# Optimization experiments

Hardware: AMD Instinct MI355X
Metric: run time of the kernel (lower is better)

## Reference

```python
import jax, jax.numpy as jnp
import numpy as np

B, N, S, NS, D = 8, 16384, 1024, 64, 128
RADIUS = 0.2
CH = [131, 128, 128, 256]  # mlp_spec after use_xyz: 128+3 input channels
EPS = 1e-5


def setup_inputs() -> dict:
    key = jax.random.key(0)
    ks = jax.random.split(key, 16)
    inp = {}
    inp["xyz"] = jax.random.uniform(ks[0], (B, N, 3), dtype=jnp.float32)
    inp["points"] = jax.random.normal(ks[1], (B, D, N), dtype=jnp.float32)
    inp["fps_idx"] = jax.random.randint(ks[2], (B, S), 0, N, dtype=jnp.int32)
    for i in range(3):
        cin, cout = CH[i], CH[i + 1]
        inp[f"W{i}"] = jax.random.normal(ks[3 + 4 * i], (cout, cin), dtype=jnp.float32) * np.float32(1.0 / np.sqrt(cin))
        inp[f"b{i}"] = jnp.zeros((cout,), dtype=jnp.float32)
        inp[f"g{i}"] = jnp.ones((cout,), dtype=jnp.float32)
        inp[f"be{i}"] = jnp.zeros((cout,), dtype=jnp.float32)
    return inp


def _ball_query(xyz, new_xyz):
    # squared distances [B, S, N] (expanded-form, same math as square_distance)
    d = (jnp.sum(new_xyz ** 2, -1, keepdims=True)
         + jnp.sum(xyz ** 2, -1)[:, None, :]
         - 2.0 * jnp.einsum('bsc,bnc->bsn', new_xyz, xyz))
    ar = jnp.arange(N, dtype=jnp.int32)[None, None, :]
    idx = jnp.where(d > RADIUS ** 2, N, ar)          # out-of-ball -> sentinel N
    idx = jnp.sort(idx, axis=-1)[:, :, :NS]          # global sort emulating top-k
    idx = jnp.where(idx == N, idx[:, :, :1], idx)    # pad with first valid neighbor
    return idx


def reference(xyz, points, fps_idx, W0, b0, g0, be0, W1, b1, g1, be1, W2, b2, g2, be2):
    feats = points.transpose(0, 2, 1)  # [B, N, D]
    new_xyz = jnp.take_along_axis(xyz, fps_idx[..., None], axis=1)  # [B, S, 3]
    idx = _ball_query(xyz, new_xyz)  # [B, S, NS]

    gather = jax.vmap(lambda a, i: a[i])  # per-batch fancy gather
    grouped_xyz = gather(xyz, idx) - new_xyz[:, :, None, :]   # [B, S, NS, 3]
    grouped_pts = gather(feats, idx)                          # [B, S, NS, D]
    x = jnp.concatenate([grouped_xyz, grouped_pts], axis=-1)  # [B, S, NS, 131]

    # SharedMLP: 1x1 Conv2d + BatchNorm (training-mode stats) + ReLU
    for W, b, g, be in ((W0, b0, g0, be0), (W1, b1, g1, be1), (W2, b2, g2, be2)):
        x = jnp.einsum('bsnc,oc->bsno', x, W) + b
        m = jnp.mean(x, axis=(0, 1, 2))
        v = jnp.var(x, axis=(0, 1, 2))
        x = jax.nn.relu(g * (x - m) * jax.lax.rsqrt(v + EPS) + be)

    new_features = jnp.max(x, axis=2).transpose(0, 2, 1)  # max over nsample -> [B, C', S]
    return new_xyz, new_features, fps_idx
```

## Files before the change

kernel.cpp:

```cpp
#include <hip/hip_runtime.h>
#include <hip/hip_bf16.h>

#define BB 8
#define NN 16384
#define SS 1024
#define NSMP 64
#define DD 128
#define R2 0.04f
#define EPSV 1e-5f

typedef _Float16 half2t __attribute__((ext_vector_type(2)));
typedef _Float16 half8t __attribute__((ext_vector_type(8)));

#define O_PT    0ull
#define O_Y0    33554432ull
#define O_Y1    167772160ull
#define O_IDX   301989888ull
#define O_MAXB  304087040ull
#define O_MINB  312475648ull
#define O_W0T   320864256ull
#define O_W1T   320931328ull
#define O_W2T   320996864ull
#define O_PS0   321127936ull
#define O_PQ0   321259008ull
#define O_PS1   321390080ull
#define O_PQ1   321521152ull
#define O_PS2   321652224ull
#define O_PQ2   321914368ull
#define O_SC0   322176512ull
#define O_SH0   322177024ull
#define O_SC1   322177536ull
#define O_SH1   322178048ull
#define O_SC2   322178560ull
#define O_SH2   322179584ull
#define WS_NEEDED 322180608ull
#define PART_BYTES 1048576ull

#define OUT_XYZ 0
#define OUT_FEAT 24576
#define OUT_FPS (24576 + 2097152)

__global__ __launch_bounds__(256) void k_transpose_pts(const float* __restrict__ pts,
                                                       _Float16* __restrict__ ptsT) {
  __shared__ float tile[32][33];
  int b = blockIdx.z;
  int n0 = blockIdx.x * 32, c0 = blockIdx.y * 32;
  int tx = threadIdx.x, ty = threadIdx.y;
#pragma unroll
  for (int k = 0; k < 4; k++) {
    int c = c0 + ty + k * 8;
    tile[ty + k * 8][tx] = pts[((size_t)b * DD + c) * NN + n0 + tx];
  }
  __syncthreads();
#pragma unroll
  for (int k = 0; k < 4; k++) {
    int n = n0 + ty + k * 8;
    ptsT[((size_t)b * NN + n) * DD + c0 + tx] = (_Float16)tile[tx][ty + k * 8];
  }
}

__global__ __launch_bounds__(256) void k_wt(const float* __restrict__ W0, const float* __restrict__ W1,
                                            const float* __restrict__ W2, float* __restrict__ W0t,
                                            float* __restrict__ W1t, float* __restrict__ W2t) {
  int id = blockIdx.x * 256 + threadIdx.x;
  if (id < 131 * 128) {
    int c = id >> 7, o = id & 127;
    int c0 = (c < 128) ? (c + 3) : (c - 128);
    W0t[id] = W0[o * 131 + c0];
  } else if (id < 131 * 128 + 128 * 128) {
    int j = id - 131 * 128;
    int c = j >> 7, o = j & 127;
    W1t[j] = W1[o * 128 + c];
  } else if (id < 131 * 128 + 128 * 128 + 128 * 256) {
    int j = id - (131 * 128 + 128 * 128);
    int c = j >> 8, o = j & 255;
    W2t[j] = W2[o * 128 + c];
  }
}

__global__ __launch_bounds__(256) void k_newxyz(const float* __restrict__ xyz, const int* __restrict__ fps,
                                                float* __restrict__ out) {
  int id = blockIdx.x * 256 + threadIdx.x;
  int fi = fps[id];
  int b = id >> 10;
  const float* p = xyz + ((size_t)b * NN + fi) * 3;
  float* o = out + OUT_XYZ + (size_t)id * 3;
  o[0] = p[0]; o[1] = p[1]; o[2] = p[2];
  out[OUT_FPS + id] = (float)fi;
}

__global__ __launch_bounds__(256) void k_ballq(const float* __restrict__ xyz, const int* __restrict__ fps,
                                               int* __restrict__ idxb) {
  int w = (blockIdx.x * 256 + threadIdx.x) >> 6;
  int lane = threadIdx.x & 63;
  int b = w >> 10;
  int fi = fps[w];
  const float* cp = xyz + ((size_t)b * NN + fi) * 3;
  float cx = cp[0], cy = cp[1], cz = cp[2];
  float A = __fadd_rn(__fadd_rn(__fmul_rn(cx, cx), __fmul_rn(cy, cy)), __fmul_rn(cz, cz));
  const float* xb = xyz + (size_t)b * NN * 3;
  int cnt = 0, firstn = -1;
  int* myidx = idxb + (size_t)w * NSMP;
  for (int nb = 0; nb < NN && cnt < NSMP; nb += 64) {
    int n = nb + lane;
    float px = xb[n * 3], py = xb[n * 3 + 1], pz = xb[n * 3 + 2];
    float Bv = __fadd_rn(__fadd_rn(__fmul_rn(px, px), __fmul_rn(py, py)), __fmul_rn(pz, pz));
    float dot = __fadd_rn(__fadd_rn(__fmul_rn(cx, px), __fmul_rn(cy, py)), __fmul_rn(cz, pz));
    float d = __fsub_rn(__fadd_rn(A, Bv), __fmul_rn(2.0f, dot));
    bool valid = !(d > R2);
    unsigned long long mask = __ballot(valid);
    if (firstn < 0 && mask) firstn = nb + __builtin_ctzll(mask);
    int prefix = __popcll(mask & ((1ull << lane) - 1ull));
    int pos = cnt + prefix;
    if (valid && pos < NSMP) myidx[pos] = n;
    cnt += __popcll(mask);
    if (cnt > NSMP) cnt = NSMP;
  }
  if (lane >= cnt) myidx[lane] = firstn;
}

__global__ __launch_bounds__(256, 2) void k_mlp0(const float* __restrict__ xyz,
                                                 const _Float16* __restrict__ ptsT,
                                                 const int* __restrict__ fps, const int* __restrict__ idxb,
                                                 const float* __restrict__ W0t, const float* __restrict__ b0,
                                                 _Float16* __restrict__ y0, float* __restrict__ psum,
                                                 float* __restrict__ psq) {
  __shared__ float xs[64 * 133];
  __shared__ float rbuf[128 * 2];
  __shared__ int smidx[64];
  __shared__ float smc[3];
  int t = threadIdx.x;
  int bs = blockIdx.x;
  int b = bs >> 10;
  if (t < 64) smidx[t] = idxb[(size_t)bs * 64 + t];
  if (t < 3) {
    int fi = fps[bs];
    smc[t] = xyz[((size_t)b * NN + fi) * 3 + t];
  }
  __syncthreads();
  {
    int row = t >> 2, q = t & 3;
    int n = smidx[row];
    const half8t* src = (const half8t*)(ptsT + ((size_t)b * NN + n) * DD);
#pragma unroll
    for (int i = 0; i < 4; i++) {
      int j = q + i * 4;
      half8t v = src[j];
      float* dstp = xs + row * 133 + j * 8;
#pragma unroll
      for (int k = 0; k < 8; k++) dstp[k] = (float)v[k];
    }
  }
  if (t < 64) {
    int n = smidx[t];
    const float* p = xyz + ((size_t)b * NN + n) * 3;
    xs[t * 133 + 128] = p[0] - smc[0];
    xs[t * 133 + 129] = p[1] - smc[1];
    xs[t * 133 + 130] = p[2] - smc[2];
  }
  __syncthreads();
  int p = t & 63;
  int obase = __builtin_amdgcn_readfirstlane((t >> 6) * 32);
  float acc[32];
#pragma unroll
  for (int oi = 0; oi < 32; oi++) acc[oi] = b0[obase + oi];
#pragma unroll 2
  for (int c = 0; c < 131; c++) {
    float xv = xs[p * 133 + c];
    const float* wr = W0t + c * 128 + obase;
#pragma unroll
    for (int oi = 0; oi < 32; oi++) acc[oi] = fmaf(xv, wr[oi], acc[oi]);
  }
  __syncthreads();
#pragma unroll
  for (int oi = 0; oi < 32; oi++) xs[p * 133 + obase + oi] = acc[oi];
  __syncthreads();
  {
    _Float16* dst = y0 + (size_t)bs * 8192;
#pragma unroll
    for (int i = 0; i < 16; i++) {
      int flat = i * 512 + 2 * t;
      int row = flat >> 7, col = flat & 127;
      half2t h;
      h[0] = (_Float16)xs[row * 133 + col];
      h[1] = (_Float16)xs[row * 133 + col + 1];
      *(half2t*)(dst + flat) = h;
    }
  }
  {
    int col = t & 127, half = t >> 7;
    float s = 0.f, q = 0.f;
#pragma unroll 4
    for (int r = half * 32; r < half * 32 + 32; r++) {
      float v = xs[r * 133 + col];
      s += v;
      q = fmaf(v, v, q);
    }
    if (half) { rbuf[col * 2] = s; rbuf[col * 2 + 1] = q; }
    __syncthreads();
    if (!half) {
      s += rbuf[col * 2];
      q += rbuf[col * 2 + 1];
      int slot = bs & 255;
      atomicAdd(&psum[col * 256 + slot], s);
      atomicAdd(&psq[col * 256 + slot], q);
    }
  }
}

__global__ __launch_bounds__(256, 2) void k_mlp1(const _Float16* __restrict__ y0,
                                                 const float* __restrict__ sc, const float* __restrict__ sh,
                                                 const float* __restrict__ W1t, const float* __restrict__ b1,
                                                 _Float16* __restrict__ y1, float* __restrict__ psum,
                                                 float* __restrict__ psq) {
  __shared__ float xs[64 * 133];
  __shared__ float rbuf[128 * 2];
  int t = threadIdx.x;
  int bs = blockIdx.x;
  {
    int colb = (2 * t) & 127;
    float a0 = sc[colb], a1 = sc[colb + 1];
    float c0 = sh[colb], c1 = sh[colb + 1];
    const _Float16* src = y0 + (size_t)bs * 8192;
#pragma unroll
    for (int i = 0; i < 16; i++) {
      int flat = i * 512 + 2 * t;
      int row = flat >> 7, col = flat & 127;
      half2t h = *(const half2t*)(src + flat);
      xs[row * 133 + col] = fmaxf(fmaf((float)h[0], a0, c0), 0.f);
      xs[row * 133 + col + 1] = fmaxf(fmaf((float)h[1], a1, c1), 0.f);
    }
  }
  __syncthreads();
  int p = t & 63;
  int obase = __builtin_amdgcn_readfirstlane((t >> 6) * 32);
  float acc[32];
#pragma unroll
  for (int oi = 0; oi < 32; oi++) acc[oi] = b1[obase + oi];
#pragma unroll 2
  for (int c = 0; c < 128; c++) {
    float xv = xs[p * 133 + c];
    const float* wr = W1t + c * 128 + obase;
#pragma unroll
    for (int oi = 0; oi < 32; oi++) acc[oi] = fmaf(xv, wr[oi], acc[oi]);
  }
  __syncthreads();
#pragma unroll
  for (int oi = 0; oi < 32; oi++) xs[p * 133 + obase + oi] = acc[oi];
  __syncthreads();
  {
    _Float16* dst = y1 + (size_t)bs * 8192;
#pragma unroll
    for (int i = 0; i < 16; i++) {
      int flat = i * 512 + 2 * t;
      int row = flat >> 7, col = flat & 127;
      half2t h;
      h[0] = (_Float16)xs[row * 133 + col];
      h[1] = (_Float16)xs[row * 133 + col + 1];
      *(half2t*)(dst + flat) = h;
    }
  }
  {
    int col = t & 127, half = t >> 7;
    float s = 0.f, q = 0.f;
#pragma unroll 4
    for (int r = half * 32; r < half * 32 + 32; r++) {
      float v = xs[r * 133 + col];
      s += v;
      q = fmaf(v, v, q);
    }
    if (half) { rbuf[col * 2] = s; rbuf[col * 2 + 1] = q; }
    __syncthreads();
    if (!half) {
      s += rbuf[col * 2];
      q += rbuf[col * 2 + 1];
      int slot = bs & 255;
      atomicAdd(&psum[col * 256 + slot], s);
      atomicAdd(&psq[col * 256 + slot], q);
    }
  }
}

__global__ __launch_bounds__(256, 2) void k_mlp2(const _Float16* __restrict__ y1,
                                                 const float* __restrict__ sc, const float* __restrict__ sh,
                                                 const float* __restrict__ W2t, const float* __restrict__ b2,
                                                 float* __restrict__ maxb, float* __restrict__ minb,
                                                 float* __restrict__ psum, float* __restrict__ psq) {
  __shared__ float xs[64 * 133];
  __shared__ float rbuf[128 * 4];
  int t = threadIdx.x;
  int bs = blockIdx.x;
  {
    int colb = (2 * t) & 127;
    float a0 = sc[colb], a1 = sc[colb + 1];
    float c0 = sh[colb], c1 = sh[colb + 1];
    const _Float16* src = y1 + (size_t)bs * 8192;
#pragma unroll
    for (int i = 0; i < 16; i++) {
      int flat = i * 512 + 2 * t;
      int row = flat >> 7, col = flat & 127;
      half2t h = *(const half2t*)(src + flat);
      xs[row * 133 + col] = fmaxf(fmaf((float)h[0], a0, c0), 0.f);
      xs[row * 133 + col + 1] = fmaxf(fmaf((float)h[1], a1, c1), 0.f);
    }
  }
  __syncthreads();
  int p = t & 63;
  int og = t >> 6;
  int obase = __builtin_amdgcn_readfirstlane(og * 64);
  float acc[64];
#pragma unroll
  for (int j = 0; j < 64; j++) acc[j] = b2[obase + j];
  for (int c = 0; c < 128; c++) {
    float xv = xs[p * 133 + c];
    const float* wr = W2t + c * 256 + obase;
#pragma unroll
    for (int j = 0; j < 64; j++) acc[j] = fmaf(xv, wr[j], acc[j]);
  }
  __syncthreads();
  for (int ph = 0; ph < 2; ph++) {
    if ((og >> 1) == ph) {
#pragma unroll
      for (int j = 0; j < 64; j++) {
        int colw = (obase + j) & 127;
        xs[p * 133 + colw] = acc[j];
      }
    }
    __syncthreads();
    {
      int col = t & 127, half = t >> 7;
      float s = 0.f, q = 0.f, mx = -3.4e38f, mn = 3.4e38f;
#pragma unroll 4
      for (int r = half * 32; r < half * 32 + 32; r++) {
        float v = xs[r * 133 + col];
        s += v;
        q = fmaf(v, v, q);
        mx = fmaxf(mx, v);
        mn = fminf(mn, v);
      }
      if (half) {
        rbuf[col * 4] = s; rbuf[col * 4 + 1] = q;
        rbuf[col * 4 + 2] = mx; rbuf[col * 4 + 3] = mn;
      }
      __syncthreads();
      if (!half) {
        s += rbuf[col * 4];
        q += rbuf[col * 4 + 1];
        mx = fmaxf(mx, rbuf[col * 4 + 2]);
        mn = fminf(mn, rbuf[col * 4 + 3]);
        int o = ph * 128 + col;
        maxb[(size_t)bs * 256 + o] = mx;
        minb[(size_t)bs * 256 + o] = mn;
        int slot = bs & 255;
        atomicAdd(&psum[o * 256 + slot], s);
        atomicAdd(&psq[o * 256 + slot], q);
      }
    }
    __syncthreads();
  }
}

__global__ __launch_bounds__(256) void k_fin(const float* __restrict__ psum, const float* __restrict__ psq,
                                             const float* __restrict__ g, const float* __restrict__ be,
                                             float* __restrict__ sc, float* __restrict__ sh, int nch) {
  int o = threadIdx.x;
  if (o >= nch) return;
  float s = 0.f, q = 0.f;
  for (int k = 0; k < 256; k++) {
    s += psum[o * 256 + k];
    q += psq[o * 256 + k];
  }
  const float inv = 1.0f / 524288.0f;
  float m = s * inv;
  float ey2 = q * inv;
  float v = fmaf(-m, m, ey2);
  v = fmaxf(v, 0.f);
  float r = rsqrtf(v + EPSV);
  float a = g[o] * r;
  sc[o] = a;
  sh[o] = fmaf(-m, a, be[o]);
}

__global__ __launch_bounds__(256) void k_out(const float* __restrict__ maxb, const float* __restrict__ minb,
                                             const float* __restrict__ sc, const float* __restrict__ sh,
                                             float* __restrict__ out) {
  int flat = blockIdx.x * 256 + threadIdx.x;
  int b = flat >> 18;
  int o = (flat >> 10) & 255;
  int s = flat & 1023;
  float a = sc[o], c_ = sh[o];
  size_t mi = ((size_t)(b * 1024 + s)) * 256 + o;
  float v = (a >= 0.f) ? maxb[mi] : minb[mi];
  out[OUT_FEAT + flat] = fmaxf(fmaf(a, v, c_), 0.f);
}

extern "C" void kernel_launch(void* const* d_in, const int* in_sizes, int n_in,
                              void* d_out, int out_size, void* d_ws, size_t ws_size,
                              hipStream_t stream) {
  const float* xyz = (const float*)d_in[0];
  const float* pts = (const float*)d_in[1];
  const int* fps = (const int*)d_in[2];
  const float* W0 = (const float*)d_in[3];
  const float* b0 = (const float*)d_in[4];
  const float* g0 = (const float*)d_in[5];
  const float* be0 = (const float*)d_in[6];
  const float* W1 = (const float*)d_in[7];
  const float* b1 = (const float*)d_in[8];
  const float* g1 = (const float*)d_in[9];
  const float* be1 = (const float*)d_in[10];
  const float* W2 = (const float*)d_in[11];
  const float* b2 = (const float*)d_in[12];
  const float* g2 = (const float*)d_in[13];
  const float* be2 = (const float*)d_in[14];
  float* out = (float*)d_out;
  char* ws = (char*)d_ws;

  k_newxyz<<<32, 256, 0, stream>>>(xyz, fps, out);
  if (ws_size < WS_NEEDED) return;

  _Float16* ptsT = (_Float16*)(ws + O_PT);
  _Float16* y0 = (_Float16*)(ws + O_Y0);
  _Float16* y1 = (_Float16*)(ws + O_Y1);
  int* idxb = (int*)(ws + O_IDX);
  float* maxbf = (float*)(ws + O_MAXB);
  float* minbf = (float*)(ws + O_MINB);
  float* W0t = (float*)(ws + O_W0T);
  float* W1t = (float*)(ws + O_W1T);
  float* W2t = (float*)(ws + O_W2T);
  float* ps0 = (float*)(ws + O_PS0);
  float* pq0 = (float*)(ws + O_PQ0);
  float* ps1 = (float*)(ws + O_PS1);
  float* pq1 = (float*)(ws + O_PQ1);
  float* ps2 = (float*)(ws + O_PS2);
  float* pq2 = (float*)(ws + O_PQ2);
  float* sc0 = (float*)(ws + O_SC0);
  float* sh0 = (float*)(ws + O_SH0);
  float* sc1 = (float*)(ws + O_SC1);
  float* sh1 = (float*)(ws + O_SH1);
  float* sc2 = (float*)(ws + O_SC2);
  float* sh2 = (float*)(ws + O_SH2);

  hipMemsetAsync(ws + O_PS0, 0, PART_BYTES, stream);
  k_transpose_pts<<<dim3(NN / 32, DD / 32, BB), dim3(32, 8), 0, stream>>>(pts, ptsT);
  k_wt<<<258, 256, 0, stream>>>(W0, W1, W2, W0t, W1t, W2t);
  k_ballq<<<2048, 256, 0, stream>>>(xyz, fps, idxb);
  k_mlp0<<<8192, 256, 0, stream>>>(xyz, ptsT, fps, idxb, W0t, b0, y0, ps0, pq0);
  k_fin<<<1, 256, 0, stream>>>(ps0, pq0, g0, be0, sc0, sh0, 128);
  k_mlp1<<<8192, 256, 0, stream>>>(y0, sc0, sh0, W1t, b1, y1, ps1, pq1);
  k_fin<<<1, 256, 0, stream>>>(ps1, pq1, g1, be1, sc1, sh1, 128);
  k_mlp2<<<8192, 256, 0, stream>>>(y1, sc1, sh1, W2t, b2, maxbf, minbf, ps2, pq2);
  k_fin<<<1, 256, 0, stream>>>(ps2, pq2, g2, be2, sc2, sh2, 256);
  k_out<<<8192, 256, 0, stream>>>(maxbf, minbf, sc2, sh2, out);
}
```

Measured before the change: 114.6 us.

## Use fp16 MFMA matrix instructions for the three pointwise MLP layers

Replaces the scalar fp32 FMA loops in the three MLP layers with 16x16x32 fp16 MFMA instructions. Activations are staged in LDS as fp16 and the weights are pre-converted to padded fp16 row-major buffers. The three xyz channels of the first layer are handled with a scalar fix-up after the MFMA part. This is meant to cut the compute-bound FMA cost, at the price of lower precision on activations, weights and the relative xyz coordinates, plus extra LDS use.

```diff
diff --git a/kernel.cpp b/kernel.cpp
--- a/kernel.cpp
+++ b/kernel.cpp
@@ -11,6 +11,7 @@
 
 typedef _Float16 half2t __attribute__((ext_vector_type(2)));
 typedef _Float16 half8t __attribute__((ext_vector_type(8)));
+typedef float f32x4 __attribute__((ext_vector_type(4)));
 
 #define O_PT    0ull
 #define O_Y0    33554432ull
@@ -60,21 +61,26 @@
 }
 
 __global__ __launch_bounds__(256) void k_wt(const float* __restrict__ W0, const float* __restrict__ W1,
-                                            const float* __restrict__ W2, float* __restrict__ W0t,
-                                            float* __restrict__ W1t, float* __restrict__ W2t) {
+                                            const float* __restrict__ W2, _Float16* __restrict__ W0h,
+                                            _Float16* __restrict__ W1h, _Float16* __restrict__ W2h) {
   int id = blockIdx.x * 256 + threadIdx.x;
-  if (id < 131 * 128) {
-    int c = id >> 7, o = id & 127;
-    int c0 = (c < 128) ? (c + 3) : (c - 128);
-    W0t[id] = W0[o * 131 + c0];
-  } else if (id < 131 * 128 + 128 * 128) {
-    int j = id - 131 * 128;
-    int c = j >> 7, o = j & 127;
-    W1t[j] = W1[o * 128 + c];
-  } else if (id < 131 * 128 + 128 * 128 + 128 * 256) {
-    int j = id - (131 * 128 + 128 * 128);
-    int c = j >> 8, o = j & 255;
-    W2t[j] = W2[o * 128 + c];
+  const int T0 = 128 * 136, T1 = 128 * 136, T2 = 256 * 136;
+  if (id < T0) {
+    int o = id / 136, c = id % 136;
+    float v = 0.f;
+    if (c < 131) {
+      int c0 = (c < 128) ? (c + 3) : (c - 128);
+      v = W0[o * 131 + c0];
+    }
+    W0h[id] = (_Float16)v;
+  } else if (id < T0 + T1) {
+    int j = id - T0;
+    int o = j / 136, c = j % 136;
+    W1h[j] = (_Float16)((c < 128) ? W1[o * 128 + c] : 0.f);
+  } else if (id < T0 + T1 + T2) {
+    int j = id - T0 - T1;
+    int o = j / 136, c = j % 136;
+    W2h[j] = (_Float16)((c < 128) ? W2[o * 128 + c] : 0.f);
   }
 }
 
@@ -122,9 +128,10 @@
 __global__ __launch_bounds__(256, 2) void k_mlp0(const float* __restrict__ xyz,
                                                  const _Float16* __restrict__ ptsT,
                                                  const int* __restrict__ fps, const int* __restrict__ idxb,
-                                                 const float* __restrict__ W0t, const float* __restrict__ b0,
+                                                 const _Float16* __restrict__ W0h, const float* __restrict__ b0,
                                                  _Float16* __restrict__ y0, float* __restrict__ psum,
                                                  float* __restrict__ psq) {
+  __shared__ _Float16 xh[64 * 136];
   __shared__ float xs[64 * 133];
   __shared__ float rbuf[128 * 2];
   __shared__ int smidx[64];
@@ -145,35 +152,62 @@
 #pragma unroll
     for (int i = 0; i < 4; i++) {
       int j = q + i * 4;
-      half8t v = src[j];
-      float* dstp = xs + row * 133 + j * 8;
-#pragma unroll
-      for (int k = 0; k < 8; k++) dstp[k] = (float)v[k];
+      *(half8t*)(xh + row * 136 + j * 8) = src[j];
     }
   }
   if (t < 64) {
     int n = smidx[t];
     const float* p = xyz + ((size_t)b * NN + n) * 3;
-    xs[t * 133 + 128] = p[0] - smc[0];
-    xs[t * 133 + 129] = p[1] - smc[1];
-    xs[t * 133 + 130] = p[2] - smc[2];
-  }
-  __syncthreads();
-  int p = t & 63;
-  int obase = __builtin_amdgcn_readfirstlane((t >> 6) * 32);
-  float acc[32];
-#pragma unroll
-  for (int oi = 0; oi < 32; oi++) acc[oi] = b0[obase + oi];
-#pragma unroll 2
-  for (int c = 0; c < 131; c++) {
-    float xv = xs[p * 133 + c];
-    const float* wr = W0t + c * 128 + obase;
-#pragma unroll
-    for (int oi = 0; oi < 32; oi++) acc[oi] = fmaf(xv, wr[oi], acc[oi]);
-  }
-  __syncthreads();
-#pragma unroll
-  for (int oi = 0; oi < 32; oi++) xs[p * 133 + obase + oi] = acc[oi];
+    xh[t * 136 + 128] = (_Float16)(p[0] - smc[0]);
+    xh[t * 136 + 129] = (_Float16)(p[1] - smc[1]);
+    xh[t * 136 + 130] = (_Float16)(p[2] - smc[2]);
+  }
+  __syncthreads();
+  int lane = t & 63;
+  int m0 = __builtin_amdgcn_readfirstlane((t >> 6) * 16);
+  int lr = lane & 15, lk = lane >> 4;
+  half8t afr[4];
+#pragma unroll
+  for (int kt = 0; kt < 4; kt++)
+    afr[kt] = *(const half8t*)(xh + (m0 + lr) * 136 + kt * 32 + lk * 8);
+  f32x4 acc[8];
+#pragma unroll
+  for (int nt = 0; nt < 8; nt++) {
+    float bv = b0[nt * 16 + lr];
+    f32x4 cv = {bv, bv, bv, bv};
+    acc[nt] = cv;
+  }
+#pragma unroll
+  for (int kt = 0; kt < 4; kt++) {
+#pragma unroll
+    for (int nt = 0; nt < 8; nt++) {
+      half8t bw = *(const half8t*)(W0h + (nt * 16 + lr) * 136 + kt * 32 + lk * 8);
+      acc[nt] = __builtin_amdgcn_mfma_f32_16x16x32_f16(afr[kt], bw, acc[nt], 0, 0, 0);
+    }
+  }
+  {
+    float xr[4][3];
+#pragma unroll
+    for (int r = 0; r < 4; r++) {
+      int m = m0 + lk * 4 + r;
+      xr[r][0] = (float)xh[m * 136 + 128];
+      xr[r][1] = (float)xh[m * 136 + 129];
+      xr[r][2] = (float)xh[m * 136 + 130];
+    }
+#pragma unroll
+    for (int nt = 0; nt < 8; nt++) {
+      const _Float16* wp = W0h + (nt * 16 + lr) * 136 + 128;
+      float w0 = (float)wp[0], w1 = (float)wp[1], w2 = (float)wp[2];
+#pragma unroll
+      for (int r = 0; r < 4; r++)
+        acc[nt][r] += xr[r][0] * w0 + xr[r][1] * w1 + xr[r][2] * w2;
+    }
+  }
+#pragma unroll
+  for (int nt = 0; nt < 8; nt++)
+#pragma unroll
+    for (int r = 0; r < 4; r++)
+      xs[(m0 + lk * 4 + r) * 133 + nt * 16 + lr] = acc[nt][r];
   __syncthreads();
   {
     _Float16* dst = y0 + (size_t)bs * 8192;
@@ -210,9 +244,10 @@
 
 __global__ __launch_bounds__(256, 2) void k_mlp1(const _Float16* __restrict__ y0,
                                                  const float* __restrict__ sc, const float* __restrict__ sh,
-                                                 const float* __restrict__ W1t, const float* __restrict__ b1,
+                                                 const _Float16* __restrict__ W1h, const float* __restrict__ b1,
                                                  _Float16* __restrict__ y1, float* __restrict__ psum,
                                                  float* __restrict__ psq) {
+  __shared__ _Float16 xh[64 * 136];
   __shared__ float xs[64 * 133];
   __shared__ float rbuf[128 * 2];
   int t = threadIdx.x;
@@ -227,26 +262,40 @@
       int flat = i * 512 + 2 * t;
       int row = flat >> 7, col = flat & 127;
       half2t h = *(const half2t*)(src + flat);
-      xs[row * 133 + col] = fmaxf(fmaf((float)h[0], a0, c0), 0.f);
-      xs[row * 133 + col + 1] = fmaxf(fmaf((float)h[1], a1, c1), 0.f);
-    }
-  }
-  __syncthreads();
-  int p = t & 63;
-  int obase = __builtin_amdgcn_readfirstlane((t >> 6) * 32);
-  float acc[32];
-#pragma unroll
-  for (int oi = 0; oi < 32; oi++) acc[oi] = b1[obase + oi];
-#pragma unroll 2
-  for (int c = 0; c < 128; c++) {
-    float xv = xs[p * 133 + c];
-    const float* wr = W1t + c * 128 + obase;
-#pragma unroll
-    for (int oi = 0; oi < 32; oi++) acc[oi] = fmaf(xv, wr[oi], acc[oi]);
-  }
-  __syncthreads();
-#pragma unroll
-  for (int oi = 0; oi < 32; oi++) xs[p * 133 + obase + oi] = acc[oi];
+      half2t o;
+      o[0] = (_Float16)fmaxf(fmaf((float)h[0], a0, c0), 0.f);
+      o[1] = (_Float16)fmaxf(fmaf((float)h[1], a1, c1), 0.f);
+      *(half2t*)(xh + row * 136 + col) = o;
+    }
+  }
+  __syncthreads();
+  int lane = t & 63;
+  int m0 = __builtin_amdgcn_readfirstlane((t >> 6) * 16);
+  int lr = lane & 15, lk = lane >> 4;
+  half8t afr[4];
+#pragma unroll
+  for (int kt = 0; kt < 4; kt++)
+    afr[kt] = *(const half8t*)(xh + (m0 + lr) * 136 + kt * 32 + lk * 8);
+  f32x4 acc[8];
+#pragma unroll
+  for (int nt = 0; nt < 8; nt++) {
+    float bv = b1[nt * 16 + lr];
+    f32x4 cv = {bv, bv, bv, bv};
+    acc[nt] = cv;
+  }
+#pragma unroll
+  for (int kt = 0; kt < 4; kt++) {
+#pragma unroll
+    for (int nt = 0; nt < 8; nt++) {
+      half8t bw = *(const half8t*)(W1h + (nt * 16 + lr) * 136 + kt * 32 + lk * 8);
+      acc[nt] = __builtin_amdgcn_mfma_f32_16x16x32_f16(afr[kt], bw, acc[nt], 0, 0, 0);
+    }
+  }
+#pragma unroll
+  for (int nt = 0; nt < 8; nt++)
+#pragma unroll
+    for (int r = 0; r < 4; r++)
+      xs[(m0 + lk * 4 + r) * 133 + nt * 16 + lr] = acc[nt][r];
   __syncthreads();
   {
     _Float16* dst = y1 + (size_t)bs * 8192;
@@ -283,9 +332,10 @@
 
 __global__ __launch_bounds__(256, 2) void k_mlp2(const _Float16* __restrict__ y1,
                                                  const float* __restrict__ sc, const float* __restrict__ sh,
-                                                 const float* __restrict__ W2t, const float* __restrict__ b2,
+                                                 const _Float16* __restrict__ W2h, const float* __restrict__ b2,
                                                  float* __restrict__ maxb, float* __restrict__ minb,
                                                  float* __restrict__ psum, float* __restrict__ psq) {
+  __shared__ _Float16 xh[64 * 136];
   __shared__ float xs[64 * 133];
   __shared__ float rbuf[128 * 4];
   int t = threadIdx.x;
@@ -300,32 +350,41 @@
       int flat = i * 512 + 2 * t;
       int row = flat >> 7, col = flat & 127;
       half2t h = *(const half2t*)(src + flat);
-      xs[row * 133 + col] = fmaxf(fmaf((float)h[0], a0, c0), 0.f);
-      xs[row * 133 + col + 1] = fmaxf(fmaf((float)h[1], a1, c1), 0.f);
-    }
-  }
-  __syncthreads();
-  int p = t & 63;
-  int og = t >> 6;
-  int obase = __builtin_amdgcn_readfirstlane(og * 64);
-  float acc[64];
-#pragma unroll
-  for (int j = 0; j < 64; j++) acc[j] = b2[obase + j];
-  for (int c = 0; c < 128; c++) {
-    float xv = xs[p * 133 + c];
-    const float* wr = W2t + c * 256 + obase;
-#pragma unroll
-    for (int j = 0; j < 64; j++) acc[j] = fmaf(xv, wr[j], acc[j]);
-  }
-  __syncthreads();
+      half2t o;
+      o[0] = (_Float16)fmaxf(fmaf((float)h[0], a0, c0), 0.f);
+      o[1] = (_Float16)fmaxf(fmaf((float)h[1], a1, c1), 0.f);
+      *(half2t*)(xh + row * 136 + col) = o;
+    }
+  }
+  __syncthreads();
+  int lane = t & 63;
+  int m0 = __builtin_amdgcn_readfirstlane((t >> 6) * 16);
+  int lr = lane & 15, lk = lane >> 4;
+  half8t afr[4];
+#pragma unroll
+  for (int kt = 0; kt < 4; kt++)
+    afr[kt] = *(const half8t*)(xh + (m0 + lr) * 136 + kt * 32 + lk * 8);
+  f32x4 acc[16];
+#pragma unroll
+  for (int nt = 0; nt < 16; nt++) {
+    float bv = b2[nt * 16 + lr];
+    f32x4 cv = {bv, bv, bv, bv};
+    acc[nt] = cv;
+  }
+#pragma unroll
+  for (int kt = 0; kt < 4; kt++) {
+#pragma unroll
+    for (int nt = 0; nt < 16; nt++) {
+      half8t bw = *(const half8t*)(W2h + (nt * 16 + lr) * 136 + kt * 32 + lk * 8);
+      acc[nt] = __builtin_amdgcn_mfma_f32_16x16x32_f16(afr[kt], bw, acc[nt], 0, 0, 0);
+    }
+  }
   for (int ph = 0; ph < 2; ph++) {
-    if ((og >> 1) == ph) {
-#pragma unroll
-      for (int j = 0; j < 64; j++) {
-        int colw = (obase + j) & 127;
-        xs[p * 133 + colw] = acc[j];
-      }
-    }
+#pragma unroll
+    for (int nt = 0; nt < 8; nt++)
+#pragma unroll
+      for (int r = 0; r < 4; r++)
+        xs[(m0 + lk * 4 + r) * 133 + nt * 16 + lr] = acc[ph * 8 + nt][r];
     __syncthreads();
     {
       int col = t & 127, half = t >> 7;
@@ -424,9 +483,9 @@
   int* idxb = (int*)(ws + O_IDX);
   float* maxbf = (float*)(ws + O_MAXB);
   float* minbf = (float*)(ws + O_MINB);
-  float* W0t = (float*)(ws + O_W0T);
-  float* W1t = (float*)(ws + O_W1T);
-  float* W2t = (float*)(ws + O_W2T);
+  _Float16* W0h = (_Float16*)(ws + O_W0T);
+  _Float16* W1h = (_Float16*)(ws + O_W1T);
+  _Float16* W2h = (_Float16*)(ws + O_W2T);
   float* ps0 = (float*)(ws + O_PS0);
   float* pq0 = (float*)(ws + O_PQ0);
   float* ps1 = (float*)(ws + O_PS1);
@@ -442,13 +501,13 @@
 
   hipMemsetAsync(ws + O_PS0, 0, PART_BYTES, stream);
   k_transpose_pts<<<dim3(NN / 32, DD / 32, BB), dim3(32, 8), 0, stream>>>(pts, ptsT);
-  k_wt<<<258, 256, 0, stream>>>(W0, W1, W2, W0t, W1t, W2t);
+  k_wt<<<272, 256, 0, stream>>>(W0, W1, W2, W0h, W1h, W2h);
   k_ballq<<<2048, 256, 0, stream>>>(xyz, fps, idxb);
-  k_mlp0<<<8192, 256, 0, stream>>>(xyz, ptsT, fps, idxb, W0t, b0, y0, ps0, pq0);
+  k_mlp0<<<8192, 256, 0, stream>>>(xyz, ptsT, fps, idxb, W0h, b0, y0, ps0, pq0);
   k_fin<<<1, 256, 0, stream>>>(ps0, pq0, g0, be0, sc0, sh0, 128);
-  k_mlp1<<<8192, 256, 0, stream>>>(y0, sc0, sh0, W1t, b1, y1, ps1, pq1);
+  k_mlp1<<<8192, 256, 0, stream>>>(y0, sc0, sh0, W1h, b1, y1, ps1, pq1);
   k_fin<<<1, 256, 0, stream>>>(ps1, pq1, g1, be1, sc1, sh1, 128);
-  k_mlp2<<<8192, 256, 0, stream>>>(y1, sc1, sh1, W2t, b2, maxbf, minbf, ps2, pq2);
+  k_mlp2<<<8192, 256, 0, stream>>>(y1, sc1, sh1, W2h, b2, maxbf, minbf, ps2, pq2);
   k_fin<<<1, 256, 0, stream>>>(ps2, pq2, g2, be2, sc2, sh2, 256);
   k_out<<<8192, 256, 0, stream>>>(maxbf, minbf, sc2, sh2, out);
 }
```

After: 116.8 us. No clear change (+2.0%).
